# Kernel optimization log

Hardware: AMD Instinct MI355X
Metric: run time of the kernel (lower is better)

Reference implementation:

```python
import jax, jax.numpy as jnp
import numpy as np

B, N, F, H, OUT = 64, 512, 128, 256, 6


def setup_inputs() -> dict:
    key = jax.random.key(0)
    ks = jax.random.split(key, 20)
    s = 0.02
    inp = {
        "x": jax.random.normal(ks[0], (B * N, F), dtype=jnp.float32),
        "edge_index": jax.random.randint(ks[1], (2, 16), 0, B * N),
        "edge_weight": jax.random.uniform(ks[2], (16,), dtype=jnp.float32),
        "batch": jnp.repeat(jnp.arange(B, dtype=jnp.int64), N),
        "sigma": jax.random.uniform(ks[3], (1,), dtype=jnp.float32),
        "Wg": s * jax.random.normal(ks[4], (F, F)), "bg": jnp.zeros((F,)),
        "Wrel0": s * jax.random.normal(ks[5], (F, H)), "Wroot0": s * jax.random.normal(ks[6], (F, H)), "brel0": jnp.zeros((H,)),
        "Wrel1": s * jax.random.normal(ks[7], (H, H)), "Wroot1": s * jax.random.normal(ks[8], (H, H)), "brel1": jnp.zeros((H,)),
        "Wrel2": s * jax.random.normal(ks[9], (H, H)), "Wroot2": s * jax.random.normal(ks[10], (H, H)), "brel2": jnp.zeros((H,)),
        "W1": s * jax.random.normal(ks[11], (H, H)), "b1": jnp.zeros((H,)),
        "Wout": s * jax.random.normal(ks[12], (H, OUT)), "bout": jnp.zeros((OUT,)),
    }
    return inp


def _forward(x, sigma, Wg, bg, Wrel0, Wroot0, brel0, Wrel1, Wroot1, brel1,
             Wrel2, Wroot2, brel2, W1, b1, Wout, bout):
    # gdmLinear
    h = x @ Wg + bg                      # [B*N, F]
    hw = h.reshape(B, N, -1)             # to_dense_batch (equal-size windows)
    # pairwise squared distances per window -> Gaussian kernel
    sq = jnp.sum(hw * hw, axis=-1)       # [B, N]
    dist = jnp.maximum(sq[:, :, None] + sq[:, None, :]
                       - 2.0 * jnp.einsum('bnf,bmf->bnm', hw, hw), 0.0)
    A = jnp.exp(-dist / (2.0 * sigma[0] ** 2))   # [B, N, N], all > 0
    A = A * (1.0 - jnp.eye(N, dtype=A.dtype))    # nonzero extraction drops self-loops

    def conv(h, Wrel, Wroot, brel):
        # GraphConv: out_i = W_rel @ sum_j A[j,i] * h_j + b_rel + W_root @ h_i
        agg = jnp.einsum('bji,bjf->bif', A, h)
        return agg @ Wrel + brel + h @ Wroot

    h = hw
    h = jax.nn.relu(conv(h, Wrel0, Wroot0, brel0))
    h = jax.nn.relu(conv(h, Wrel1, Wroot1, brel1))
    h = conv(h, Wrel2, Wroot2, brel2)
    g = jnp.mean(h, axis=1)              # global_mean_pool (equal-size graphs)
    g = jax.nn.relu(g @ W1 + b1)
    return g @ Wout + bout               # [B, OUT]


def reference(x, edge_index, edge_weight, batch, sigma, Wg, bg,
              Wrel0, Wroot0, brel0, Wrel1, Wroot1, brel1,
              Wrel2, Wroot2, brel2, W1, b1, Wout, bout):
    # edge_index / edge_weight / batch inputs are recomputed internally by GdmGNN
    return _forward(x, sigma, Wg, bg, Wrel0, Wroot0, brel0, Wrel1, Wroot1, brel1,
                    Wrel2, Wroot2, brel2, W1, b1, Wout, bout)
```

## Files before the change

kernel.cpp:

```cpp
#include <hip/hip_runtime.h>
#include <math.h>

#define Bsz 64
#define Nn 512
#define Ff 128
#define Hh 256
#define OUTD 6
#define MTOT (Bsz * Nn)

typedef __bf16 bf16x8 __attribute__((ext_vector_type(8)));
typedef float f32x4 __attribute__((ext_vector_type(4)));
typedef int int4v __attribute__((ext_vector_type(4)));
typedef unsigned short ushort4v __attribute__((ext_vector_type(4)));

__device__ __forceinline__ unsigned short f2bf(float f) {
    unsigned u = __float_as_uint(f);
    u += 0x7FFFu + ((u >> 16) & 1u);
    return (unsigned short)(u >> 16);
}
__device__ __forceinline__ float bf2f(unsigned short s) {
    return __uint_as_float(((unsigned)s) << 16);
}

#define SWZ(r) (((r) ^ ((r) >> 2)) & 3)

__device__ __forceinline__ void async_ld16(const unsigned short* g, unsigned short* l) {
    __builtin_amdgcn_global_load_lds(
        (const __attribute__((address_space(1))) void*)g,
        (__attribute__((address_space(3))) void*)l,
        16, 0, 0);
}

#define LDH 40
#define TSZ (128 * 32)

__global__ __launch_bounds__(512) void gemm_ah(
    const unsigned short* __restrict__ A0, const unsigned short* __restrict__ B0T,
    unsigned short* __restrict__ C,
    int Ntot, int K0,
    long strideA0, long strideB0, long strideC, int tilesPerRow)
{
    int id = blockIdx.x;
    int bz = id & 63;
    int t = id >> 6;
    int bx = t % tilesPerRow;
    int by = t / tilesPerRow;

    A0 += (long)bz * strideA0;
    B0T += (long)bz * strideB0;
    C += (long)bz * strideC;

    __shared__ unsigned short As[2 * TSZ];
    __shared__ unsigned short Bs[2 * TSZ];

    int tid = threadIdx.x;
    int lane = tid & 63;
    int wave = tid >> 6;
    int quad = lane >> 4, l16 = lane & 15;
    int wm = (wave >> 1) * 32, wn = (wave & 1) * 64;
    int m0 = bx * 128, n0 = by * 128;

    int sr = lane >> 2, sc = lane & 3;

    int T = K0 >> 5;

    f32x4 acc[2][4] = {};

    auto issue = [&](int g) {
        int kk = g << 5;
        unsigned short* Ad = As + (g & 1) * TSZ;
        unsigned short* Bd = Bs + (g & 1) * TSZ;
        int r = wave * 16 + sr;
        int c = sc ^ SWZ(r);
        async_ld16(A0 + (long)(m0 + r) * K0 + kk + c * 8, Ad + (wave * 16) * 32);
        async_ld16(B0T + (long)(n0 + r) * K0 + kk + c * 8, Bd + (wave * 16) * 32);
    };

    issue(0);
    for (int g = 0; g < T; ++g) {
        __syncthreads();
        if (g + 1 < T) issue(g + 1);
        const unsigned short* Ab = As + (g & 1) * TSZ;
        const unsigned short* Bb = Bs + (g & 1) * TSZ;
        bf16x8 af[2], bfr[4];
        #pragma unroll
        for (int i = 0; i < 2; ++i) {
            int r = wm + i * 16 + l16;
            af[i] = *(const bf16x8*)&Ab[r * 32 + (quad ^ SWZ(r)) * 8];
        }
        #pragma unroll
        for (int j = 0; j < 4; ++j) {
            int r = wn + j * 16 + l16;
            bfr[j] = *(const bf16x8*)&Bb[r * 32 + (quad ^ SWZ(r)) * 8];
        }
        #pragma unroll
        for (int i = 0; i < 2; ++i)
            #pragma unroll
            for (int j = 0; j < 4; ++j)
                acc[i][j] = __builtin_amdgcn_mfma_f32_16x16x32_bf16(
                    af[i], bfr[j], acc[i][j], 0, 0, 0);
    }

    #pragma unroll
    for (int i = 0; i < 2; ++i) {
        int mb = m0 + wm + i * 16 + quad * 4;
        #pragma unroll
        for (int j = 0; j < 4; ++j) {
            int n = n0 + wn + j * 16 + l16;
            f32x4 v = acc[i][j];
            C[(long)(mb + 0) * Ntot + n] = f2bf(v[0]);
            C[(long)(mb + 1) * Ntot + n] = f2bf(v[1]);
            C[(long)(mb + 2) * Ntot + n] = f2bf(v[2]);
            C[(long)(mb + 3) * Ntot + n] = f2bf(v[3]);
        }
    }
}

__global__ __launch_bounds__(512) void dense_t(
    const unsigned short* __restrict__ A0, const unsigned short* __restrict__ B0T,
    const unsigned short* __restrict__ A1, const unsigned short* __restrict__ B1T,
    const float* __restrict__ bias,
    unsigned short* __restrict__ outB, unsigned short* __restrict__ outT,
    int K0, int K1, int relu)
{
    int m0 = blockIdx.x * 128;
    int n0 = blockIdx.y * 128;

    __shared__ unsigned short As[2 * TSZ];
    __shared__ unsigned short Bs[2 * TSZ];

    int tid = threadIdx.x;
    int lane = tid & 63;
    int wave = tid >> 6;
    int quad = lane >> 4, l16 = lane & 15;
    int wm = (wave >> 1) * 32, wn = (wave & 1) * 64;

    int sr = lane >> 2, sc = lane & 3;

    int T0 = K0 >> 5, T1 = K1 >> 5;
    int T = T0 + T1;

    f32x4 acc[2][4] = {};

    auto issue = [&](int g) {
        const unsigned short* Ag; const unsigned short* Bg; int Kg, kk;
        if (g < T0) { Ag = A0; Bg = B0T; Kg = K0; kk = g << 5; }
        else        { Ag = A1; Bg = B1T; Kg = K1; kk = (g - T0) << 5; }
        unsigned short* Ad = As + (g & 1) * TSZ;
        unsigned short* Bd = Bs + (g & 1) * TSZ;
        int r = wave * 16 + sr;
        int c = sc ^ SWZ(r);
        async_ld16(Ag + (long)(m0 + r) * Kg + kk + c * 8, Ad + (wave * 16) * 32);
        async_ld16(Bg + (long)(n0 + r) * Kg + kk + c * 8, Bd + (wave * 16) * 32);
    };

    issue(0);
    for (int g = 0; g < T; ++g) {
        __syncthreads();
        if (g + 1 < T) issue(g + 1);
        const unsigned short* Ab = As + (g & 1) * TSZ;
        const unsigned short* Bb = Bs + (g & 1) * TSZ;
        bf16x8 af[2], bfr[4];
        #pragma unroll
        for (int i = 0; i < 2; ++i) {
            int r = wm + i * 16 + l16;
            af[i] = *(const bf16x8*)&Ab[r * 32 + (quad ^ SWZ(r)) * 8];
        }
        #pragma unroll
        for (int j = 0; j < 4; ++j) {
            int r = wn + j * 16 + l16;
            bfr[j] = *(const bf16x8*)&Bb[r * 32 + (quad ^ SWZ(r)) * 8];
        }
        #pragma unroll
        for (int i = 0; i < 2; ++i)
            #pragma unroll
            for (int j = 0; j < 4; ++j)
                acc[i][j] = __builtin_amdgcn_mfma_f32_16x16x32_bf16(
                    af[i], bfr[j], acc[i][j], 0, 0, 0);
    }

    #pragma unroll
    for (int i = 0; i < 2; ++i) {
        int of = m0 + wm + i * 16 + quad * 4;
        float b0 = bias[of + 0], b1 = bias[of + 1];
        float b2 = bias[of + 2], b3 = bias[of + 3];
        #pragma unroll
        for (int j = 0; j < 4; ++j) {
            int node = n0 + wn + j * 16 + l16;
            f32x4 v = acc[i][j];
            float o0 = v[0] + b0, o1 = v[1] + b1, o2 = v[2] + b2, o3 = v[3] + b3;
            if (relu) {
                o0 = fmaxf(o0, 0.f); o1 = fmaxf(o1, 0.f);
                o2 = fmaxf(o2, 0.f); o3 = fmaxf(o3, 0.f);
            }
            ushort4v p;
            p[0] = f2bf(o0); p[1] = f2bf(o1); p[2] = f2bf(o2); p[3] = f2bf(o3);
            *(ushort4v*)&outB[(long)node * Hh + of] = p;
            if (outT) {
                long base = ((long)(node >> 9) * Hh) * 512 + (node & 511);
                outT[base + (long)(of + 0) * 512] = p[0];
                outT[base + (long)(of + 1) * 512] = p[1];
                outT[base + (long)(of + 2) * 512] = p[2];
                outT[base + (long)(of + 3) * 512] = p[3];
            }
        }
    }
}

__global__ __launch_bounds__(256) void prep_h0(
    const float* __restrict__ x, const float* __restrict__ Wg,
    const float* __restrict__ bg,
    const float* __restrict__ Wrel0, const float* __restrict__ Wroot0,
    const float* __restrict__ Wrel1, const float* __restrict__ Wroot1,
    unsigned short* __restrict__ T0, unsigned short* __restrict__ T1,
    unsigned short* __restrict__ T2, unsigned short* __restrict__ T3,
    unsigned short* __restrict__ WgT,
    float* __restrict__ w,
    unsigned short* __restrict__ h0b, unsigned short* __restrict__ h0T,
    float* __restrict__ sqv)
{
    if (blockIdx.x < 960) {
        int idx = blockIdx.x * 256 + threadIdx.x;
        if (idx >= 212992) { w[idx - 212992] = 0.f; return; }
        if (idx >= 196608) {
            int e = idx - 196608;
            int o = e >> 7, i = e & 127;
            WgT[e] = f2bf(Wg[(long)i * 128 + o]);
            return;
        }
        const float* src; unsigned short* dst; int kin; int e;
        if      (idx <  32768) { src = Wrel0;  dst = T0; kin = 128; e = idx; }
        else if (idx <  65536) { src = Wroot0; dst = T1; kin = 128; e = idx - 32768; }
        else if (idx < 131072) { src = Wrel1;  dst = T2; kin = 256; e = idx - 65536; }
        else                   { src = Wroot1; dst = T3; kin = 256; e = idx - 131072; }
        int o = (kin == 128) ? (e >> 7) : (e >> 8);
        int i = e & (kin - 1);
        dst[e] = f2bf(src[(long)i * 256 + o]);
        return;
    }

    __shared__ unsigned short As[128 * LDH];
    __shared__ unsigned short Bs[128 * LDH];
    __shared__ float rsq[128];

    int tid = threadIdx.x;
    int lane = tid & 63;
    int wave = tid >> 6;
    int quad = lane >> 4, l16 = lane & 15;
    int wm = (wave >> 1) * 64, wn = (wave & 1) * 64;
    int m0 = (blockIdx.x - 960) * 128;

    f32x4 acc[4][4] = {};

    for (int k0 = 0; k0 < Ff; k0 += 32) {
        __syncthreads();
        #pragma unroll
        for (int l = 0; l < 2; ++l) {
            int idx = tid + l * 256;
            int r = idx >> 2, ch = idx & 3;
            const float* px = x + (long)(m0 + r) * Ff + k0 + ch * 8;
            float4 xa = *(const float4*)px;
            float4 xb = *(const float4*)(px + 4);
            ushort4v pa, pb;
            pa[0] = f2bf(xa.x); pa[1] = f2bf(xa.y); pa[2] = f2bf(xa.z); pa[3] = f2bf(xa.w);
            pb[0] = f2bf(xb.x); pb[1] = f2bf(xb.y); pb[2] = f2bf(xb.z); pb[3] = f2bf(xb.w);
            *(ushort4v*)&As[r * LDH + ch * 8] = pa;
            *(ushort4v*)&As[r * LDH + ch * 8 + 4] = pb;
            int kk = k0 + ch * 8;
            ushort4v qa, qb;
            #pragma unroll
            for (int u = 0; u < 4; ++u) qa[u] = f2bf(Wg[(long)(kk + u) * 128 + r]);
            #pragma unroll
            for (int u = 0; u < 4; ++u) qb[u] = f2bf(Wg[(long)(kk + 4 + u) * 128 + r]);
            *(ushort4v*)&Bs[r * LDH + ch * 8] = qa;
            *(ushort4v*)&Bs[r * LDH + ch * 8 + 4] = qb;
        }
        __syncthreads();
        bf16x8 af[4], bfr[4];
        #pragma unroll
        for (int i = 0; i < 4; ++i)
            af[i] = *(const bf16x8*)&As[(wm + i * 16 + l16) * LDH + quad * 8];
        #pragma unroll
        for (int j = 0; j < 4; ++j)
            bfr[j] = *(const bf16x8*)&Bs[(wn + j * 16 + l16) * LDH + quad * 8];
        #pragma unroll
        for (int i = 0; i < 4; ++i)
            #pragma unroll
            for (int j = 0; j < 4; ++j)
                acc[i][j] = __builtin_amdgcn_mfma_f32_16x16x32_bf16(
                    af[i], bfr[j], acc[i][j], 0, 0, 0);
    }

    if (tid < 128) rsq[tid] = 0.f;
    __syncthreads();

    #pragma unroll
    for (int i = 0; i < 4; ++i) {
        int lrow = wm + i * 16 + quad * 4;
        int mb = m0 + lrow;
        float rp0 = 0.f, rp1 = 0.f, rp2 = 0.f, rp3 = 0.f;
        #pragma unroll
        for (int j = 0; j < 4; ++j) {
            int n = wn + j * 16 + l16;
            f32x4 v = acc[i][j];
            float bv = bg[n];
            unsigned short s0 = f2bf(v[0] + bv), s1 = f2bf(v[1] + bv);
            unsigned short s2 = f2bf(v[2] + bv), s3 = f2bf(v[3] + bv);
            h0b[(long)(mb + 0) * Ff + n] = s0;
            h0b[(long)(mb + 1) * Ff + n] = s1;
            h0b[(long)(mb + 2) * Ff + n] = s2;
            h0b[(long)(mb + 3) * Ff + n] = s3;
            ushort4v p; p[0] = s0; p[1] = s1; p[2] = s2; p[3] = s3;
            long ti = ((long)(mb >> 9) * Ff + n) * 512 + (mb & 511);
            *(ushort4v*)&h0T[ti] = p;
            float f0 = bf2f(s0), f1 = bf2f(s1), f2 = bf2f(s2), f3 = bf2f(s3);
            rp0 += f0 * f0; rp1 += f1 * f1; rp2 += f2 * f2; rp3 += f3 * f3;
        }
        #pragma unroll
        for (int m = 1; m < 16; m <<= 1) {
            rp0 += __shfl_xor(rp0, m);
            rp1 += __shfl_xor(rp1, m);
            rp2 += __shfl_xor(rp2, m);
            rp3 += __shfl_xor(rp3, m);
        }
        if (l16 == 0) {
            atomicAdd(&rsq[lrow + 0], rp0);
            atomicAdd(&rsq[lrow + 1], rp1);
            atomicAdd(&rsq[lrow + 2], rp2);
            atomicAdd(&rsq[lrow + 3], rp3);
        }
    }
    __syncthreads();
    if (tid < 128) sqv[m0 + tid] = rsq[tid];
}

__global__ __launch_bounds__(512) void gram_A_mfma(
    const unsigned short* __restrict__ h0b, const float* __restrict__ sqv,
    const float* __restrict__ sigma, unsigned short* __restrict__ Aout,
    float* __restrict__ w)
{
    int id = blockIdx.x;
    int b = id & 63;
    int t = id >> 6;
    int i0 = (t & 3) * 128, j0 = (t >> 2) * 128;

    const unsigned short* H = h0b + (long)b * Nn * Ff;
    const float* SQ = sqv + (long)b * Nn;
    unsigned short* Ab = Aout + (long)b * Nn * Nn;

    __shared__ unsigned short Is[2 * TSZ];
    __shared__ unsigned short Js[2 * TSZ];
    __shared__ float rsum[128];

    int tid = threadIdx.x;
    int lane = tid & 63;
    int wave = tid >> 6;
    int quad = lane >> 4, l16 = lane & 15;
    int wm = (wave >> 1) * 32, wn = (wave & 1) * 64;

    int sr = lane >> 2, sc = lane & 3;

    f32x4 acc[2][4] = {};

    auto issue = [&](int g) {
        int kk = g << 5;
        unsigned short* Id = Is + (g & 1) * TSZ;
        unsigned short* Jd = Js + (g & 1) * TSZ;
        int r = wave * 16 + sr;
        int c = sc ^ SWZ(r);
        async_ld16(H + (long)(i0 + r) * Ff + kk + c * 8, Id + (wave * 16) * 32);
        async_ld16(H + (long)(j0 + r) * Ff + kk + c * 8, Jd + (wave * 16) * 32);
    };

    issue(0);
    for (int g = 0; g < (Ff >> 5); ++g) {
        __syncthreads();
        if (g + 1 < (Ff >> 5)) issue(g + 1);
        const unsigned short* Ib = Is + (g & 1) * TSZ;
        const unsigned short* Jb = Js + (g & 1) * TSZ;
        bf16x8 af[2], bfr[4];
        #pragma unroll
        for (int i = 0; i < 2; ++i) {
            int r = wm + i * 16 + l16;
            af[i] = *(const bf16x8*)&Ib[r * 32 + (quad ^ SWZ(r)) * 8];
        }
        #pragma unroll
        for (int j = 0; j < 4; ++j) {
            int r = wn + j * 16 + l16;
            bfr[j] = *(const bf16x8*)&Jb[r * 32 + (quad ^ SWZ(r)) * 8];
        }
        #pragma unroll
        for (int i = 0; i < 2; ++i)
            #pragma unroll
            for (int j = 0; j < 4; ++j)
                acc[i][j] = __builtin_amdgcn_mfma_f32_16x16x32_bf16(
                    af[i], bfr[j], acc[i][j], 0, 0, 0);
    }

    if (tid < 128) rsum[tid] = 0.f;
    __syncthreads();

    float s = sigma[0];
    float inv2s2 = 1.0f / (2.0f * s * s);
    #pragma unroll
    for (int i = 0; i < 2; ++i) {
        int lrow = wm + i * 16 + quad * 4;
        int rb = i0 + lrow;
        float rs0 = 0.f, rs1 = 0.f, rs2 = 0.f, rs3 = 0.f;
        #pragma unroll
        for (int j = 0; j < 4; ++j) {
            int c = j0 + wn + j * 16 + l16;
            float sqc = SQ[c];
            f32x4 v = acc[i][j];
            ushort4v pk;
            float av[4];
            #pragma unroll
            for (int r4 = 0; r4 < 4; ++r4) {
                int r = rb + r4;
                float d = fmaxf(SQ[r] + sqc - 2.0f * v[r4], 0.0f);
                unsigned short a = (r == c) ? (unsigned short)0
                                            : f2bf(__expf(-d * inv2s2));
                pk[r4] = a;
                av[r4] = bf2f(a);
            }
            *(ushort4v*)&Ab[(long)c * Nn + rb] = pk;
            rs0 += av[0]; rs1 += av[1]; rs2 += av[2]; rs3 += av[3];
        }
        #pragma unroll
        for (int m = 1; m < 16; m <<= 1) {
            rs0 += __shfl_xor(rs0, m);
            rs1 += __shfl_xor(rs1, m);
            rs2 += __shfl_xor(rs2, m);
            rs3 += __shfl_xor(rs3, m);
        }
        if (l16 == 0) {
            atomicAdd(&rsum[lrow + 0], rs0);
            atomicAdd(&rsum[lrow + 1], rs1);
            atomicAdd(&rsum[lrow + 2], rs2);
            atomicAdd(&rsum[lrow + 3], rs3);
        }
    }
    __syncthreads();
    if (tid < 128) atomicAdd(&w[(long)b * Nn + i0 + tid], rsum[tid]);
}

__global__ __launch_bounds__(256) void reduce_h2(
    const unsigned short* __restrict__ h2b, const float* __restrict__ w,
    float* __restrict__ vpart, float* __restrict__ mpart)
{
    int b = blockIdx.x;
    int jc = blockIdx.y;
    int c = threadIdx.x;
    const unsigned short* H = h2b + ((long)b * Nn + jc * 64) * Hh + c;
    const float* wp = w + (long)b * Nn + jc * 64;
    float vp = 0.f, mp = 0.f;
    #pragma unroll 4
    for (int j = 0; j < 64; ++j) {
        float val = bf2f(H[(long)j * Hh]);
        mp += val;
        vp += wp[j] * val;
    }
    long o = ((long)b * 8 + jc) * Hh + c;
    vpart[o] = vp;
    mpart[o] = mp;
}

__global__ __launch_bounds__(256) void head_kernel(
    const float* __restrict__ vpart, const float* __restrict__ mpart,
    const float* __restrict__ Wrel2, const float* __restrict__ Wroot2,
    const float* __restrict__ brel2,
    const float* __restrict__ W1, const float* __restrict__ b1,
    const float* __restrict__ Wout, const float* __restrict__ bout,
    float* __restrict__ out)
{
    int b = blockIdx.x;
    int j = threadIdx.x;
    __shared__ float vs[Hh], ms[Hh], gs[Hh], g2[Hh];
    float vp = 0.f, mp = 0.f;
    #pragma unroll
    for (int p = 0; p < 8; ++p) {
        long o = ((long)b * 8 + p) * Hh + j;
        vp += vpart[o];
        mp += mpart[o];
    }
    vs[j] = vp * (1.0f / (float)Nn);
    ms[j] = mp * (1.0f / (float)Nn);
    __syncthreads();
    float s = brel2[j];
    for (int c = 0; c < Hh; ++c)
        s += vs[c] * Wrel2[c * Hh + j] + ms[c] * Wroot2[c * Hh + j];
    gs[j] = s;
    __syncthreads();
    float t = b1[j];
    for (int k = 0; k < Hh; ++k) t += gs[k] * W1[k * Hh + j];
    g2[j] = fmaxf(t, 0.f);
    __syncthreads();
    if (j < OUTD) {
        float s2 = bout[j];
        for (int k = 0; k < Hh; ++k) s2 += g2[k] * Wout[k * OUTD + j];
        out[b * OUTD + j] = s2;
    }
}

extern "C" void kernel_launch(void* const* d_in, const int* in_sizes, int n_in,
                              void* d_out, int out_size, void* d_ws, size_t ws_size,
                              hipStream_t stream) {
    const float* x      = (const float*)d_in[0];
    const float* sigma  = (const float*)d_in[4];
    const float* Wg     = (const float*)d_in[5];
    const float* bg     = (const float*)d_in[6];
    const float* Wrel0  = (const float*)d_in[7];
    const float* Wroot0 = (const float*)d_in[8];
    const float* brel0  = (const float*)d_in[9];
    const float* Wrel1  = (const float*)d_in[10];
    const float* Wroot1 = (const float*)d_in[11];
    const float* brel1  = (const float*)d_in[12];
    const float* Wrel2  = (const float*)d_in[13];
    const float* Wroot2 = (const float*)d_in[14];
    const float* brel2  = (const float*)d_in[15];
    const float* W1     = (const float*)d_in[16];
    const float* b1     = (const float*)d_in[17];
    const float* Wout   = (const float*)d_in[18];
    const float* bout   = (const float*)d_in[19];
    float* out = (float*)d_out;

    char* ws = (char*)d_ws;
    unsigned short* WgT  = (unsigned short*)(ws + 0);
    unsigned short* h0b  = (unsigned short*)(ws + 16777216);
    unsigned short* h0T  = (unsigned short*)(ws + 25165824);
    float*          sq   = (float*)(ws + 33554432);
    unsigned short* Aadj = (unsigned short*)(ws + 33685504);
    unsigned short* agg  = (unsigned short*)(ws + 67239936);
    unsigned short* h1b  = (unsigned short*)(ws + 84017152);
    unsigned short* h1T  = (unsigned short*)(ws + 100794368);
    unsigned short* h2b  = (unsigned short*)(ws + 117571584);
    unsigned short* WrelT0  = (unsigned short*)(ws + 167903232);
    unsigned short* WrootT0 = (unsigned short*)(ws + 167968768);
    unsigned short* WrelT1  = (unsigned short*)(ws + 168034304);
    unsigned short* WrootT1 = (unsigned short*)(ws + 168165376);
    float*          w     = (float*)(ws + 168558592);
    float*          vpart = (float*)(ws + 168689664);
    float*          mpart = (float*)(ws + 169213952);

    prep_h0<<<1216, 256, 0, stream>>>(x, Wg, bg, Wrel0, Wroot0, Wrel1, Wroot1,
                                      WrelT0, WrootT0, WrelT1, WrootT1, WgT,
                                      w, h0b, h0T, sq);

    gram_A_mfma<<<dim3(16 * Bsz, 1, 1), 512, 0, stream>>>(h0b, sq, sigma, Aadj, w);

    gemm_ah<<<dim3(4 * Bsz, 1, 1), 512, 0, stream>>>(
        Aadj, h0T, agg, Ff, Nn,
        (long)Nn * Nn, (long)Ff * Nn, (long)Nn * Ff, 4);
    dense_t<<<dim3(2, MTOT / 128), 512, 0, stream>>>(
        WrelT0, agg, WrootT0, h0b, brel0, h1b, h1T, Ff, Ff, 1);

    gemm_ah<<<dim3(8 * Bsz, 1, 1), 512, 0, stream>>>(
        Aadj, h1T, agg, Hh, Nn,
        (long)Nn * Nn, (long)Hh * Nn, (long)Nn * Hh, 4);
    dense_t<<<dim3(2, MTOT / 128), 512, 0, stream>>>(
        WrelT1, agg, WrootT1, h1b, brel1, h2b, nullptr, Hh, Hh, 1);

    reduce_h2<<<dim3(Bsz, 8), 256, 0, stream>>>(h2b, w, vpart, mpart);
    head_kernel<<<Bsz, 256, 0, stream>>>(vpart, mpart, Wrel2, Wroot2, brel2,
                                         W1, b1, Wout, bout, out);
}
```

Before: 234.0 us.

## Exploit adjacency symmetry: compute upper-triangle Gram tiles and mirror writes

The Gram/adjacency kernel now computes only the 10 upper-triangular 128x128 tiles per graph instead of all 16. Each off-diagonal tile writes both itself and its transpose, and accumulates column sums into the degree vector. The aggregation GEMM swaps operand roles (H^T as the M side, adjacency rows as the N side) so its output stores become packed 4-element vectors. This reduces MFMA and exp work in the Gram stage, but the mirrored writes are scalar, strided 2-byte stores that may be poorly coalesced.

```diff
diff --git a/kernel.cpp b/kernel.cpp
--- a/kernel.cpp
+++ b/kernel.cpp
@@ -35,20 +35,19 @@
 #define TSZ (128 * 32)
 
 __global__ __launch_bounds__(512) void gemm_ah(
-    const unsigned short* __restrict__ A0, const unsigned short* __restrict__ B0T,
-    unsigned short* __restrict__ C,
-    int Ntot, int K0,
-    long strideA0, long strideB0, long strideC, int tilesPerRow)
+    const unsigned short* __restrict__ HT, const unsigned short* __restrict__ Arows,
+    unsigned short* __restrict__ agg,
+    int F, long strideHT, long strideA, long strideC, int mTiles)
 {
     int id = blockIdx.x;
     int bz = id & 63;
     int t = id >> 6;
-    int bx = t % tilesPerRow;
-    int by = t / tilesPerRow;
-
-    A0 += (long)bz * strideA0;
-    B0T += (long)bz * strideB0;
-    C += (long)bz * strideC;
+    int bx = t % mTiles;
+    int by = t / mTiles;
+
+    HT += (long)bz * strideHT;
+    Arows += (long)bz * strideA;
+    agg += (long)bz * strideC;
 
     __shared__ unsigned short As[2 * TSZ];
     __shared__ unsigned short Bs[2 * TSZ];
@@ -62,8 +61,6 @@
 
     int sr = lane >> 2, sc = lane & 3;
 
-    int T = K0 >> 5;
-
     f32x4 acc[2][4] = {};
 
     auto issue = [&](int g) {
@@ -72,14 +69,14 @@
         unsigned short* Bd = Bs + (g & 1) * TSZ;
         int r = wave * 16 + sr;
         int c = sc ^ SWZ(r);
-        async_ld16(A0 + (long)(m0 + r) * K0 + kk + c * 8, Ad + (wave * 16) * 32);
-        async_ld16(B0T + (long)(n0 + r) * K0 + kk + c * 8, Bd + (wave * 16) * 32);
+        async_ld16(HT + (long)(m0 + r) * Nn + kk + c * 8, Ad + (wave * 16) * 32);
+        async_ld16(Arows + (long)(n0 + r) * Nn + kk + c * 8, Bd + (wave * 16) * 32);
     };
 
     issue(0);
-    for (int g = 0; g < T; ++g) {
+    for (int g = 0; g < (Nn >> 5); ++g) {
         __syncthreads();
-        if (g + 1 < T) issue(g + 1);
+        if (g + 1 < (Nn >> 5)) issue(g + 1);
         const unsigned short* Ab = As + (g & 1) * TSZ;
         const unsigned short* Bb = Bs + (g & 1) * TSZ;
         bf16x8 af[2], bfr[4];
@@ -103,15 +100,14 @@
 
     #pragma unroll
     for (int i = 0; i < 2; ++i) {
-        int mb = m0 + wm + i * 16 + quad * 4;
-        #pragma unroll
-        for (int j = 0; j < 4; ++j) {
-            int n = n0 + wn + j * 16 + l16;
+        int f = m0 + wm + i * 16 + quad * 4;
+        #pragma unroll
+        for (int j = 0; j < 4; ++j) {
+            int node = n0 + wn + j * 16 + l16;
             f32x4 v = acc[i][j];
-            C[(long)(mb + 0) * Ntot + n] = f2bf(v[0]);
-            C[(long)(mb + 1) * Ntot + n] = f2bf(v[1]);
-            C[(long)(mb + 2) * Ntot + n] = f2bf(v[2]);
-            C[(long)(mb + 3) * Ntot + n] = f2bf(v[3]);
+            ushort4v p;
+            p[0] = f2bf(v[0]); p[1] = f2bf(v[1]); p[2] = f2bf(v[2]); p[3] = f2bf(v[3]);
+            *(ushort4v*)&agg[(long)node * F + f] = p;
         }
     }
 }
@@ -339,10 +335,13 @@
     const float* __restrict__ sigma, unsigned short* __restrict__ Aout,
     float* __restrict__ w)
 {
+    const int ti_[10] = {0,0,0,0,1,1,1,2,2,3};
+    const int tj_[10] = {0,1,2,3,1,2,3,2,3,3};
     int id = blockIdx.x;
     int b = id & 63;
-    int t = id >> 6;
-    int i0 = (t & 3) * 128, j0 = (t >> 2) * 128;
+    int tt = id >> 6;
+    int i0 = ti_[tt] * 128, j0 = tj_[tt] * 128;
+    bool offdiag = (i0 != j0);
 
     const unsigned short* H = h0b + (long)b * Nn * Ff;
     const float* SQ = sqv + (long)b * Nn;
@@ -351,6 +350,7 @@
     __shared__ unsigned short Is[2 * TSZ];
     __shared__ unsigned short Js[2 * TSZ];
     __shared__ float rsum[128];
+    __shared__ float csum[128];
 
     int tid = threadIdx.x;
     int lane = tid & 63;
@@ -397,11 +397,12 @@
                     af[i], bfr[j], acc[i][j], 0, 0, 0);
     }
 
-    if (tid < 128) rsum[tid] = 0.f;
+    if (tid < 128) { rsum[tid] = 0.f; csum[tid] = 0.f; }
     __syncthreads();
 
     float s = sigma[0];
     float inv2s2 = 1.0f / (2.0f * s * s);
+    float cj[4] = {0.f, 0.f, 0.f, 0.f};
     #pragma unroll
     for (int i = 0; i < 2; ++i) {
         int lrow = wm + i * 16 + quad * 4;
@@ -424,6 +425,13 @@
                 av[r4] = bf2f(a);
             }
             *(ushort4v*)&Ab[(long)c * Nn + rb] = pk;
+            if (offdiag) {
+                Ab[(long)(rb + 0) * Nn + c] = pk[0];
+                Ab[(long)(rb + 1) * Nn + c] = pk[1];
+                Ab[(long)(rb + 2) * Nn + c] = pk[2];
+                Ab[(long)(rb + 3) * Nn + c] = pk[3];
+                cj[j] += av[0] + av[1] + av[2] + av[3];
+            }
             rs0 += av[0]; rs1 += av[1]; rs2 += av[2]; rs3 += av[3];
         }
         #pragma unroll
@@ -440,8 +448,23 @@
             atomicAdd(&rsum[lrow + 3], rs3);
         }
     }
-    __syncthreads();
-    if (tid < 128) atomicAdd(&w[(long)b * Nn + i0 + tid], rsum[tid]);
+    if (offdiag) {
+        #pragma unroll
+        for (int j = 0; j < 4; ++j) {
+            cj[j] += __shfl_xor(cj[j], 16);
+            cj[j] += __shfl_xor(cj[j], 32);
+        }
+        if (quad == 0) {
+            #pragma unroll
+            for (int j = 0; j < 4; ++j)
+                atomicAdd(&csum[wn + j * 16 + l16], cj[j]);
+        }
+    }
+    __syncthreads();
+    if (tid < 128) {
+        atomicAdd(&w[(long)b * Nn + i0 + tid], rsum[tid]);
+        if (offdiag) atomicAdd(&w[(long)b * Nn + j0 + tid], csum[tid]);
+    }
 }
 
 __global__ __launch_bounds__(256) void reduce_h2(
@@ -546,17 +569,17 @@
                                       WrelT0, WrootT0, WrelT1, WrootT1, WgT,
                                       w, h0b, h0T, sq);
 
-    gram_A_mfma<<<dim3(16 * Bsz, 1, 1), 512, 0, stream>>>(h0b, sq, sigma, Aadj, w);
+    gram_A_mfma<<<dim3(10 * Bsz, 1, 1), 512, 0, stream>>>(h0b, sq, sigma, Aadj, w);
 
     gemm_ah<<<dim3(4 * Bsz, 1, 1), 512, 0, stream>>>(
-        Aadj, h0T, agg, Ff, Nn,
-        (long)Nn * Nn, (long)Ff * Nn, (long)Nn * Ff, 4);
+        h0T, Aadj, agg, Ff,
+        (long)Ff * Nn, (long)Nn * Nn, (long)Nn * Ff, 1);
     dense_t<<<dim3(2, MTOT / 128), 512, 0, stream>>>(
         WrelT0, agg, WrootT0, h0b, brel0, h1b, h1T, Ff, Ff, 1);
 
     gemm_ah<<<dim3(8 * Bsz, 1, 1), 512, 0, stream>>>(
-        Aadj, h1T, agg, Hh, Nn,
-        (long)Nn * Nn, (long)Hh * Nn, (long)Nn * Hh, 4);
+        h1T, Aadj, agg, Hh,
+        (long)Hh * Nn, (long)Nn * Nn, (long)Nn * Hh, 2);
     dense_t<<<dim3(2, MTOT / 128), 512, 0, stream>>>(
         WrelT1, agg, WrootT1, h1b, brel1, h2b, nullptr, Hh, Hh, 1);
 
```

Measured after the change: 235.8 us. Within noise of the previous version (+0.8%).
